# Kernel optimization log

Measured on AMD Instinct MI355X. Metric: run time of the kernel, lower is better.

The kernel has to match this reference:

```python
import jax, jax.numpy as jnp
import numpy as np

# ---- problem dims ----
B, S, C, H, W = 4, 8, 3, 256, 256
P = 68          # keypoints (self.points)
DS = 4          # detector downsample
WIN = 8
STEPS = 10      # Gauss-Newton iterations per frame pair
EPS = 1e-6
GRAY_W = jnp.array([0.299, 0.587, 0.114], dtype=jnp.float32)

# window offsets [K,2] in (x,y)
_rng = jnp.arange(-WIN, WIN + 1, dtype=jnp.float32)
_OFF = jnp.stack(jnp.meshgrid(_rng, _rng, indexing='xy'), -1).reshape(-1, 2)


def setup_inputs() -> dict:
    key = jax.random.key(0)
    k1, k2 = jax.random.split(key)
    inputs = jax.random.normal(k1, (B, S, C, H, W), dtype=jnp.float32)
    Wdet = jax.random.normal(k2, (P, C, 3, 3), dtype=jnp.float32) * 0.1
    bdet = jnp.zeros((P,), dtype=jnp.float32)
    return {"inputs": inputs, "Wdet": Wdet, "bdet": bdet}


def _bilinear(img, xy):
    # img [H,W]; xy [...,2] in (x,y) pixel coords -> sampled values [...]
    x = jnp.clip(xy[..., 0], 0.0, W - 1.001)
    y = jnp.clip(xy[..., 1], 0.0, H - 1.001)
    x0 = jnp.floor(x); y0 = jnp.floor(y)
    wx = x - x0; wy = y - y0
    x0i = x0.astype(jnp.int32); y0i = y0.astype(jnp.int32)
    x1i = jnp.minimum(x0i + 1, W - 1); y1i = jnp.minimum(y0i + 1, H - 1)
    v00 = img[y0i, x0i]; v01 = img[y0i, x1i]
    v10 = img[y1i, x0i]; v11 = img[y1i, x1i]
    return (1 - wy) * ((1 - wx) * v00 + wx * v01) + wy * ((1 - wx) * v10 + wx * v11)


def _grad_xy(img):
    # central differences with edge replication
    px = jnp.pad(img, ((0, 0), (1, 1)), mode='edge')
    py = jnp.pad(img, ((1, 1), (0, 0)), mode='edge')
    gx = (px[:, 2:] - px[:, :-2]) * 0.5
    gy = (py[2:, :] - py[:-2, :]) * 0.5
    return gx, gy


def _lk_track(old, new, pts):
    # one Lucas-Kanade tracking step: old/new [H,W] gray, pts [P,2] -> [P,2]
    gx, gy = _grad_xy(old)
    pos0 = pts[:, None, :] + _OFF[None]            # [P,K,2]
    I0 = _bilinear(old, pos0)                      # [P,K] template patch
    Ix = _bilinear(gx, pos0)
    Iy = _bilinear(gy, pos0)
    Gxx = (Ix * Ix).sum(-1); Gxy = (Ix * Iy).sum(-1); Gyy = (Iy * Iy).sum(-1)
    det = Gxx * Gyy - Gxy * Gxy + EPS
    Ginv = jnp.stack([jnp.stack([Gyy, -Gxy], -1),
                      jnp.stack([-Gxy, Gxx], -1)], -2) / det[:, None, None]  # [P,2,2]

    def step(i, v):
        I1 = _bilinear(new, pos0 + v[:, None, :])  # [P,K]
        err = I0 - I1
        b = jnp.stack([(err * Ix).sum(-1), (err * Iy).sum(-1)], -1)  # [P,2]
        return v + jnp.einsum('pij,pj->pi', Ginv, b)

    v = jax.lax.fori_loop(0, STEPS, step, jnp.zeros_like(pts))
    return pts + v


def _lk_forward_backward(gray, locs):
    # gray [S,H,W], locs [S,P,2] -> nextPts, fbackPts, backPts each [S,P,2]
    def f(pts, frames):
        o, n = frames
        q = _lk_track(o, n, pts)
        return q, q

    # forward: track detector locs of frame 0 through the sequence
    _, fout = jax.lax.scan(f, locs[0], (gray[:-1], gray[1:]))
    nextPts = jnp.concatenate([locs[:1], fout], 0)
    ro, rn = gray[1:][::-1], gray[:-1][::-1]
    # forward-backward: track the forward end point back to frame 0
    _, fbout = jax.lax.scan(f, nextPts[-1], (ro, rn))
    fbackPts = jnp.concatenate([nextPts[-1:], fbout], 0)[::-1]
    # backward: track detector locs of last frame back through the sequence
    _, bout = jax.lax.scan(f, locs[-1], (ro, rn))
    backPts = jnp.concatenate([locs[-1:], bout], 0)[::-1]
    return nextPts, fbackPts, backPts


def _detector(x, Wdet, bdet):
    # x [N,C,H,W] -> heatmaps [N,P,H/DS,W/DS], locs [N,P,2] (pixel coords), scores [N,P]
    hm = jax.lax.conv_general_dilated(
        x, Wdet, window_strides=(DS, DS), padding='SAME',
        dimension_numbers=('NCHW', 'OIHW', 'NCHW')) + bdet[None, :, None, None]
    N, _, Hd, Wd = hm.shape
    flat = hm.reshape(N, P, Hd * Wd)
    prob = jax.nn.softmax(flat, axis=-1)
    ys, xs = jnp.meshgrid(jnp.arange(Hd, dtype=hm.dtype),
                          jnp.arange(Wd, dtype=hm.dtype), indexing='ij')
    ex = (prob * xs.reshape(-1)).sum(-1) * DS   # soft-argmax, upscaled to input px
    ey = (prob * ys.reshape(-1)).sum(-1) * DS
    locs = jnp.stack([ex, ey], -1)
    scos = flat.max(-1)
    return hm, locs, scos


def reference(inputs, Wdet, bdet):
    x = inputs.reshape(B * S, C, H, W)
    hm, locs, scos = _detector(x, Wdet, bdet)
    heatmaps = hm.reshape(B, S, P, H // DS, W // DS)
    batch_locs = locs.reshape(B, S, P, 2)
    batch_scos = scos.reshape(B, S, P)
    gray = jnp.einsum('bschw,c->bshw', inputs, GRAY_W)  # [B,S,H,W]
    nextPts, fbackPts, backPts = jax.vmap(_lk_forward_backward)(gray, batch_locs)
    return heatmaps, batch_locs, batch_scos, nextPts, fbackPts, backPts
```

## Files before the change

kernel.cpp:

```cpp
#include <hip/hip_runtime.h>
#include <math.h>

namespace {
constexpr int Bn = 4, Sn = 8, Cn = 3, Himg = 256, Wimg = 256;
constexpr int Pn = 68, DS = 4, WIN = 8, STEPS = 10;
constexpr int HWi = Himg * Wimg;
constexpr int NIMG = Bn * Sn;
constexpr int HD = Himg / DS, WD = Wimg / DS;
constexpr int Kwin = (2 * WIN + 1) * (2 * WIN + 1);
}

__global__ __launch_bounds__(256) void gray2_kernel(const float* __restrict__ in,
                                                    float* __restrict__ gray,
                                                    float* __restrict__ sh) {
    int idx = blockIdx.x * blockDim.x + threadIdx.x;
    int total = NIMG * HWi / 4;
    if (idx >= total) return;
    int img = idx / (HWi / 4);
    int off = idx % (HWi / 4);
    const float* base = in + (size_t)img * 3 * HWi;
    float4 c0 = ((const float4*)(base))[off];
    float4 c1 = ((const float4*)(base + HWi))[off];
    float4 c2 = ((const float4*)(base + 2 * HWi))[off];
    float4 g;
    g.x = 0.299f * c0.x + 0.587f * c1.x + 0.114f * c2.x;
    g.y = 0.299f * c0.y + 0.587f * c1.y + 0.114f * c2.y;
    g.z = 0.299f * c0.z + 0.587f * c1.z + 0.114f * c2.z;
    g.w = 0.299f * c0.w + 0.587f * c1.w + 0.114f * c2.w;
    float gn = 0.f;
    int gi = idx * 4 + 4;
    if (gi < NIMG * HWi) {
        int i2 = gi / HWi;
        int o2 = gi % HWi;
        const float* b2 = in + (size_t)i2 * 3 * HWi;
        gn = 0.299f * b2[o2] + 0.587f * b2[o2 + HWi] + 0.114f * b2[o2 + 2 * HWi];
    }
    ((float4*)(gray + (size_t)img * HWi))[off] = g;
    float4 s;
    s.x = g.y; s.y = g.z; s.z = g.w; s.w = gn;
    ((float4*)(sh + (size_t)img * HWi))[off] = s;
}

__global__ __launch_bounds__(256) void conv_kernel(const float* __restrict__ x,
                                                   const float* __restrict__ Wdet,
                                                   const float* __restrict__ bdet,
                                                   float* __restrict__ hm) {
    __shared__ float wsh[Pn * 27];
    __shared__ float bsh[Pn];
    __shared__ float insh[3][3][Wimg];
    int n = blockIdx.x >> 6;
    int oy = blockIdx.x & 63;
    int tid = threadIdx.x;
    for (int t = tid; t < Pn * 27; t += 256) wsh[t] = Wdet[t];
    if (tid < Pn) bsh[tid] = bdet[tid];
    for (int t = tid; t < 3 * 3 * Wimg; t += 256) {
        int c = t / (3 * Wimg);
        int r = (t / Wimg) % 3;
        int col = t % Wimg;
        insh[c][r][col] = x[(size_t)n * 3 * HWi + (size_t)c * HWi + (oy * 4 + r) * Wimg + col];
    }
    __syncthreads();
    int ox = tid & 63;
    int wid = tid >> 6;
    float in_reg[27];
    #pragma unroll
    for (int c = 0; c < 3; c++)
        #pragma unroll
        for (int ky = 0; ky < 3; ky++)
            #pragma unroll
            for (int kx = 0; kx < 3; kx++)
                in_reg[c * 9 + ky * 3 + kx] = insh[c][ky][ox * 4 + kx];
    #pragma unroll
    for (int i = 0; i < 17; i++) {
        int p = wid + i * 4;
        const float* w = &wsh[p * 27];
        float acc = bsh[p];
        #pragma unroll
        for (int j = 0; j < 27; j++) acc += w[j] * in_reg[j];
        hm[(size_t)n * Pn * 4096 + (size_t)p * 4096 + oy * 64 + ox] = acc;
    }
}

__global__ __launch_bounds__(256) void smax_kernel(const float* __restrict__ hm,
                                                   float* __restrict__ locs,
                                                   float* __restrict__ scos) {
    int row = blockIdx.x;
    const float4* r = (const float4*)(hm + (size_t)row * 4096);
    int tid = threadIdx.x;
    float v[16];
    #pragma unroll
    for (int j = 0; j < 4; j++) {
        float4 q = r[tid + 256 * j];
        v[4 * j + 0] = q.x; v[4 * j + 1] = q.y; v[4 * j + 2] = q.z; v[4 * j + 3] = q.w;
    }
    float m = v[0];
    #pragma unroll
    for (int i = 1; i < 16; i++) m = fmaxf(m, v[i]);
    __shared__ float redm[4];
    #pragma unroll
    for (int o = 32; o; o >>= 1) m = fmaxf(m, __shfl_xor(m, o, 64));
    int wid = tid >> 6, lane = tid & 63;
    if (lane == 0) redm[wid] = m;
    __syncthreads();
    m = fmaxf(fmaxf(redm[0], redm[1]), fmaxf(redm[2], redm[3]));
    float s = 0.f, sx = 0.f, sy = 0.f;
    #pragma unroll
    for (int j = 0; j < 4; j++) {
        #pragma unroll
        for (int q = 0; q < 4; q++) {
            int e = (tid + 256 * j) * 4 + q;
            float ev = expf(v[4 * j + q] - m);
            s += ev;
            sx += ev * (float)(e & 63);
            sy += ev * (float)(e >> 6);
        }
    }
    #pragma unroll
    for (int o = 32; o; o >>= 1) {
        s  += __shfl_xor(s, o, 64);
        sx += __shfl_xor(sx, o, 64);
        sy += __shfl_xor(sy, o, 64);
    }
    __shared__ float reds[3][4];
    if (lane == 0) { reds[0][wid] = s; reds[1][wid] = sx; reds[2][wid] = sy; }
    __syncthreads();
    if (tid == 0) {
        float S_ = reds[0][0] + reds[0][1] + reds[0][2] + reds[0][3];
        float SX = reds[1][0] + reds[1][1] + reds[1][2] + reds[1][3];
        float SY = reds[2][0] + reds[2][1] + reds[2][2] + reds[2][3];
        locs[(size_t)row * 2 + 0] = SX / S_ * 4.0f;
        locs[(size_t)row * 2 + 1] = SY / S_ * 4.0f;
        scos[row] = m;
    }
}

template <int CTRL>
__device__ inline float dpp_add(float v) {
    int t = __builtin_amdgcn_update_dpp(0, __builtin_bit_cast(int, v), CTRL, 0xF, 0xF, true);
    return v + __builtin_bit_cast(float, t);
}

__device__ inline float wredw(float v) {
    v = dpp_add<0x111>(v);
    v = dpp_add<0x112>(v);
    v = dpp_add<0x114>(v);
    v = dpp_add<0x118>(v);
    v = dpp_add<0x142>(v);
    v = dpp_add<0x143>(v);
    int s = __builtin_amdgcn_readlane(__builtin_bit_cast(int, v), 63);
    return __builtin_bit_cast(float, s);
}

__device__ void lk_track_pair(const float* __restrict__ oldI, const float* __restrict__ oldS,
                              const float* __restrict__ newI, const float* __restrict__ newS,
                              float& px, float& py, const float* dxs, const float* dys,
                              float s4w) {
    const float XM = (float)(Wimg - 1.001);
    const float YM = (float)(Himg - 1.001);
    float I0[5], Ix[5], Iy[5], qx[5], qy[5];
    {
        float wx[5], wy[5];
        const float* pb[5];
        int xe[5], am[5], a0[5], a1[5], ap[5], xm[5], xp[5];
        #pragma unroll
        for (int j = 0; j < 5; j++) {
            qx[j] = px + dxs[j];
            qy[j] = py + dys[j];
            float x = fminf(fmaxf(qx[j], 0.0f), XM);
            float y = fminf(fmaxf(qy[j], 0.0f), YM);
            float x0f = floorf(x), y0f = floorf(y);
            wx[j] = x - x0f; wy[j] = y - y0f;
            int xi = (int)x0f, yi = (int)y0f;
            xe[j] = xi & ~1;
            pb[j] = (xi & 1) ? oldS : oldI;
            xm[j] = max(xi - 1, 0);
            xp[j] = min(xi + 2, Wimg - 1);
            a0[j] = yi * Wimg;
            a1[j] = a0[j] + Wimg;
            am[j] = max(yi - 1, 0) * Wimg;
            ap[j] = min(yi + 2, Himg - 1) * Wimg;
        }
        float2 Pm[5], P0[5], P1[5], Pp[5];
        float c0m[5], c0p[5], c1m[5], c1p[5];
        #pragma unroll
        for (int j = 0; j < 5; j++) {
            Pm[j] = *(const float2*)(pb[j] + am[j] + xe[j]);
            P0[j] = *(const float2*)(pb[j] + a0[j] + xe[j]);
            P1[j] = *(const float2*)(pb[j] + a1[j] + xe[j]);
            Pp[j] = *(const float2*)(pb[j] + ap[j] + xe[j]);
            c0m[j] = oldI[a0[j] + xm[j]];
            c0p[j] = oldI[a0[j] + xp[j]];
            c1m[j] = oldI[a1[j] + xm[j]];
            c1p[j] = oldI[a1[j] + xp[j]];
        }
        #pragma unroll
        for (int j = 0; j < 5; j++) {
            float m0 = Pm[j].x, m1 = Pm[j].y;
            float c00 = P0[j].x, c01 = P0[j].y;
            float c10 = P1[j].x, c11 = P1[j].y;
            float p0 = Pp[j].x, p1 = Pp[j].y;
            float u = 1.0f - wx[j], t = 1.0f - wy[j];
            I0[j] = t * (u * c00 + wx[j] * c01) + wy[j] * (u * c10 + wx[j] * c11);
            float gx00 = 0.5f * (c01 - c0m[j]);
            float gx01 = 0.5f * (c0p[j] - c00);
            float gx10 = 0.5f * (c11 - c1m[j]);
            float gx11 = 0.5f * (c1p[j] - c10);
            Ix[j] = t * (u * gx00 + wx[j] * gx01) + wy[j] * (u * gx10 + wx[j] * gx11);
            float gy00 = 0.5f * (c10 - m0);
            float gy01 = 0.5f * (c11 - m1);
            float gy10 = 0.5f * (p0 - c00);
            float gy11 = 0.5f * (p1 - c01);
            Iy[j] = t * (u * gy00 + wx[j] * gy01) + wy[j] * (u * gy10 + wx[j] * gy11);
        }
        Ix[4] *= s4w;
        Iy[4] *= s4w;
    }
    float gxx = 0.f, gxy = 0.f, gyy = 0.f;
    #pragma unroll
    for (int j = 0; j < 5; j++) { gxx += Ix[j] * Ix[j]; gxy += Ix[j] * Iy[j]; gyy += Iy[j] * Iy[j]; }
    gxx = wredw(gxx); gxy = wredw(gxy); gyy = wredw(gyy);
    float det = gxx * gyy - gxy * gxy + 1e-6f;
    float A = gyy / det, Bv = -gxy / det, D = gxx / det;
    float vx = 0.f, vy = 0.f;
    for (int it = 0; it < STEPS; ++it) {
        float fx[5], fy[5];
        const float* pb[5];
        int aa[5];
        #pragma unroll
        for (int j = 0; j < 5; j++) {
            float x = fminf(fmaxf(qx[j] + vx, 0.0f), XM);
            float y = fminf(fmaxf(qy[j] + vy, 0.0f), YM);
            float x0f = floorf(x), y0f = floorf(y);
            fx[j] = x - x0f; fy[j] = y - y0f;
            int xi = (int)x0f, yi = (int)y0f;
            pb[j] = (xi & 1) ? newS : newI;
            aa[j] = yi * Wimg + (xi & ~1);
        }
        float2 R0[5], R1[5];
        #pragma unroll
        for (int j = 0; j < 5; j++) {
            R0[j] = *(const float2*)(pb[j] + aa[j]);
            R1[j] = *(const float2*)(pb[j] + aa[j] + Wimg);
        }
        float bx = 0.f, by = 0.f;
        #pragma unroll
        for (int j = 0; j < 5; j++) {
            float u = 1.0f - fx[j], t = 1.0f - fy[j];
            float I1 = t * (u * R0[j].x + fx[j] * R0[j].y) + fy[j] * (u * R1[j].x + fx[j] * R1[j].y);
            float err = I0[j] - I1;
            bx += err * Ix[j];
            by += err * Iy[j];
        }
        bx = wredw(bx); by = wredw(by);
        vx += A * bx + Bv * by;
        vy += Bv * bx + D * by;
    }
    px += vx; py += vy;
}

__global__ __launch_bounds__(64) void lk_pair_kernel(const float* __restrict__ gray,
                                                     const float* __restrict__ sh,
                                                     const float* __restrict__ locs,
                                                     float* __restrict__ nextPts,
                                                     float* __restrict__ fbackPts,
                                                     float* __restrict__ backPts) {
    int g = blockIdx.x;
    int typ = g / (Bn * Pn);
    int r = g % (Bn * Pn);
    int b = r / Pn;
    int p = r % Pn;
    int lane = threadIdx.x;
    const float* G = gray + (size_t)b * Sn * HWi;
    const float* S = sh + (size_t)b * Sn * HWi;
    float dxs[5], dys[5];
    #pragma unroll
    for (int j = 0; j < 4; j++) {
        int k = lane + 64 * j;
        dxs[j] = (float)(k % 17 - 8);
        dys[j] = (float)(k / 17 - 8);
    }
    {
        int k4 = (lane < Kwin - 256) ? 256 + lane : 256;
        dxs[4] = (float)(k4 % 17 - 8);
        dys[4] = (float)(k4 / 17 - 8);
    }
    float s4w = (lane < Kwin - 256) ? 1.0f : 0.0f;
    auto LIDX = [&](int s) { return (((size_t)b * Sn + s) * Pn + p) * 2; };
    if (typ == 0) {
        float px = locs[LIDX(0)], py = locs[LIDX(0) + 1];
        if (lane == 0) { nextPts[LIDX(0)] = px; nextPts[LIDX(0) + 1] = py; }
        for (int s = 0; s < 7; s++) {
            lk_track_pair(G + s * HWi, S + s * HWi, G + (s + 1) * HWi, S + (s + 1) * HWi,
                          px, py, dxs, dys, s4w);
            if (lane == 0) { nextPts[LIDX(s + 1)] = px; nextPts[LIDX(s + 1) + 1] = py; }
        }
        if (lane == 0) { fbackPts[LIDX(7)] = px; fbackPts[LIDX(7) + 1] = py; }
        for (int i = 0; i < 7; i++) {
            lk_track_pair(G + (7 - i) * HWi, S + (7 - i) * HWi, G + (6 - i) * HWi, S + (6 - i) * HWi,
                          px, py, dxs, dys, s4w);
            if (lane == 0) { fbackPts[LIDX(6 - i)] = px; fbackPts[LIDX(6 - i) + 1] = py; }
        }
    } else {
        float px = locs[LIDX(7)], py = locs[LIDX(7) + 1];
        if (lane == 0) { backPts[LIDX(7)] = px; backPts[LIDX(7) + 1] = py; }
        for (int i = 0; i < 7; i++) {
            lk_track_pair(G + (7 - i) * HWi, S + (7 - i) * HWi, G + (6 - i) * HWi, S + (6 - i) * HWi,
                          px, py, dxs, dys, s4w);
            if (lane == 0) { backPts[LIDX(6 - i)] = px; backPts[LIDX(6 - i) + 1] = py; }
        }
    }
}

__device__ inline float px_fly(const float* __restrict__ im, int idx) {
    return 0.299f * im[idx] + 0.587f * im[idx + HWi] + 0.114f * im[idx + 2 * HWi];
}

__device__ void lk_track_fly(const float* __restrict__ oldI, const float* __restrict__ newI,
                             float& px, float& py, const float* dxs, const float* dys,
                             float s4w) {
    const float XM = (float)(Wimg - 1.001);
    const float YM = (float)(Himg - 1.001);
    float I0[5], Ix[5], Iy[5], qx[5], qy[5];
    {
        float wx[5], wy[5];
        int am[5], a0[5], a1[5], ap[5], xm[5], x0[5], x1[5], xp[5];
        #pragma unroll
        for (int j = 0; j < 5; j++) {
            qx[j] = px + dxs[j]; qy[j] = py + dys[j];
            float x = fminf(fmaxf(qx[j], 0.0f), XM);
            float y = fminf(fmaxf(qy[j], 0.0f), YM);
            float x0f = floorf(x), y0f = floorf(y);
            wx[j] = x - x0f; wy[j] = y - y0f;
            int xi = (int)x0f, yi = (int)y0f;
            x0[j] = xi; x1[j] = min(xi + 1, Wimg - 1);
            xm[j] = max(xi - 1, 0); xp[j] = min(xi + 2, Wimg - 1);
            a0[j] = yi * Wimg;
            a1[j] = min(yi + 1, Himg - 1) * Wimg;
            am[j] = max(yi - 1, 0) * Wimg;
            ap[j] = min(yi + 2, Himg - 1) * Wimg;
        }
        #pragma unroll
        for (int j = 0; j < 5; j++) {
            float m0 = px_fly(oldI, am[j] + x0[j]), m1 = px_fly(oldI, am[j] + x1[j]);
            float c0m = px_fly(oldI, a0[j] + xm[j]), c00 = px_fly(oldI, a0[j] + x0[j]);
            float c01 = px_fly(oldI, a0[j] + x1[j]), c0p = px_fly(oldI, a0[j] + xp[j]);
            float c1m = px_fly(oldI, a1[j] + xm[j]), c10 = px_fly(oldI, a1[j] + x0[j]);
            float c11 = px_fly(oldI, a1[j] + x1[j]), c1p = px_fly(oldI, a1[j] + xp[j]);
            float p0 = px_fly(oldI, ap[j] + x0[j]), p1 = px_fly(oldI, ap[j] + x1[j]);
            float u = 1.0f - wx[j], t = 1.0f - wy[j];
            I0[j] = t * (u * c00 + wx[j] * c01) + wy[j] * (u * c10 + wx[j] * c11);
            Ix[j] = t * (u * 0.5f * (c01 - c0m) + wx[j] * 0.5f * (c0p - c00))
                  + wy[j] * (u * 0.5f * (c11 - c1m) + wx[j] * 0.5f * (c1p - c10));
            Iy[j] = t * (u * 0.5f * (c10 - m0) + wx[j] * 0.5f * (c11 - m1))
                  + wy[j] * (u * 0.5f * (p0 - c00) + wx[j] * 0.5f * (p1 - c01));
        }
        Ix[4] *= s4w; Iy[4] *= s4w;
    }
    float gxx = 0.f, gxy = 0.f, gyy = 0.f;
    #pragma unroll
    for (int j = 0; j < 5; j++) { gxx += Ix[j] * Ix[j]; gxy += Ix[j] * Iy[j]; gyy += Iy[j] * Iy[j]; }
    gxx = wredw(gxx); gxy = wredw(gxy); gyy = wredw(gyy);
    float det = gxx * gyy - gxy * gxy + 1e-6f;
    float A = gyy / det, Bv = -gxy / det, D = gxx / det;
    float vx = 0.f, vy = 0.f;
    for (int it = 0; it < STEPS; ++it) {
        float bx = 0.f, by = 0.f;
        #pragma unroll
        for (int j = 0; j < 5; j++) {
            float x = fminf(fmaxf(qx[j] + vx, 0.0f), XM);
            float y = fminf(fmaxf(qy[j] + vy, 0.0f), YM);
            float x0f = floorf(x), y0f = floorf(y);
            float fxx = x - x0f, fyy = y - y0f;
            int xi = (int)x0f, yi = (int)y0f;
            int ad = yi * Wimg + xi;
            float v00 = px_fly(newI, ad), v01 = px_fly(newI, ad + 1);
            float v10 = px_fly(newI, ad + Wimg), v11 = px_fly(newI, ad + Wimg + 1);
            float u = 1.0f - fxx, t = 1.0f - fyy;
            float I1 = t * (u * v00 + fxx * v01) + fyy * (u * v10 + fxx * v11);
            float err = I0[j] - I1;
            bx += err * Ix[j];
            by += err * Iy[j];
        }
        bx = wredw(bx); by = wredw(by);
        vx += A * bx + Bv * by;
        vy += Bv * bx + D * by;
    }
    px += vx; py += vy;
}

__global__ __launch_bounds__(64) void lk_fly_kernel(const float* __restrict__ in,
                                                    const float* __restrict__ locs,
                                                    float* __restrict__ nextPts,
                                                    float* __restrict__ fbackPts,
                                                    float* __restrict__ backPts) {
    constexpr size_t FS = (size_t)3 * HWi;
    int g = blockIdx.x;
    int typ = g / (Bn * Pn);
    int r = g % (Bn * Pn);
    int b = r / Pn;
    int p = r % Pn;
    int lane = threadIdx.x;
    const float* G = in + (size_t)b * Sn * FS;
    float dxs[5], dys[5];
    #pragma unroll
    for (int j = 0; j < 4; j++) {
        int k = lane + 64 * j;
        dxs[j] = (float)(k % 17 - 8);
        dys[j] = (float)(k / 17 - 8);
    }
    {
        int k4 = (lane < Kwin - 256) ? 256 + lane : 256;
        dxs[4] = (float)(k4 % 17 - 8);
        dys[4] = (float)(k4 / 17 - 8);
    }
    float s4w = (lane < Kwin - 256) ? 1.0f : 0.0f;
    auto LIDX = [&](int s) { return (((size_t)b * Sn + s) * Pn + p) * 2; };
    if (typ == 0) {
        float px = locs[LIDX(0)], py = locs[LIDX(0) + 1];
        if (lane == 0) { nextPts[LIDX(0)] = px; nextPts[LIDX(0) + 1] = py; }
        for (int s = 0; s < 7; s++) {
            lk_track_fly(G + s * FS, G + (s + 1) * FS, px, py, dxs, dys, s4w);
            if (lane == 0) { nextPts[LIDX(s + 1)] = px; nextPts[LIDX(s + 1) + 1] = py; }
        }
        if (lane == 0) { fbackPts[LIDX(7)] = px; fbackPts[LIDX(7) + 1] = py; }
        for (int i = 0; i < 7; i++) {
            lk_track_fly(G + (7 - i) * FS, G + (6 - i) * FS, px, py, dxs, dys, s4w);
            if (lane == 0) { fbackPts[LIDX(6 - i)] = px; fbackPts[LIDX(6 - i) + 1] = py; }
        }
    } else {
        float px = locs[LIDX(7)], py = locs[LIDX(7) + 1];
        if (lane == 0) { backPts[LIDX(7)] = px; backPts[LIDX(7) + 1] = py; }
        for (int i = 0; i < 7; i++) {
            lk_track_fly(G + (7 - i) * FS, G + (6 - i) * FS, px, py, dxs, dys, s4w);
            if (lane == 0) { backPts[LIDX(6 - i)] = px; backPts[LIDX(6 - i) + 1] = py; }
        }
    }
}

extern "C" void kernel_launch(void* const* d_in, const int* in_sizes, int n_in,
                              void* d_out, int out_size, void* d_ws, size_t ws_size,
                              hipStream_t stream) {
    const float* inputs = (const float*)d_in[0];
    const float* Wdet = (const float*)d_in[1];
    const float* bdet = (const float*)d_in[2];
    float* out = (float*)d_out;

    const size_t N_hm = (size_t)Bn * Sn * Pn * HD * WD;
    const size_t N_pts = (size_t)Bn * Sn * Pn * 2;
    float* hm = out;
    float* locs = out + N_hm;
    float* scos = locs + N_pts;
    float* nextPts = scos + (size_t)Bn * Sn * Pn;
    float* fbackPts = nextPts + N_pts;
    float* backPts = fbackPts + N_pts;

    conv_kernel<<<NIMG * 64, 256, 0, stream>>>(inputs, Wdet, bdet, hm);
    smax_kernel<<<NIMG * Pn, 256, 0, stream>>>(hm, locs, scos);

    const size_t gray_elems = (size_t)NIMG * HWi;
    if (ws_size >= 2 * gray_elems * sizeof(float)) {
        float* gray = (float*)d_ws;
        float* sh = gray + gray_elems;
        gray2_kernel<<<(NIMG * HWi / 4 + 255) / 256, 256, 0, stream>>>(inputs, gray, sh);
        lk_pair_kernel<<<2 * Bn * Pn, 64, 0, stream>>>(gray, sh, locs, nextPts, fbackPts, backPts);
    } else {
        lk_fly_kernel<<<2 * Bn * Pn, 64, 0, stream>>>(inputs, locs, nextPts, fbackPts, backPts);
    }
}
```

Measured before the change: 121.7 us.

## Stage per-frame 40x40 LK patches in LDS instead of shifted gray copies

The gray kernel no longer writes a second, one-pixel-shifted gray image, which halves the workspace traffic. Each LK track step now cooperatively loads a 40x40 window of the old and new frames into shared memory. Template, gradient and Gauss-Newton samples are then read from LDS, with a fallback to global reads when the displaced window leaves the patch. This trades global gathers for one bulk patch load and two barriers per frame pair. The fly path also gains edge clamping on the +1 neighbours.

New measurement: 125.3 us. 1.03x slower.

```diff
diff --git a/kernel.cpp b/kernel.cpp
--- a/kernel.cpp
+++ b/kernel.cpp
@@ -8,11 +8,13 @@
 constexpr int NIMG = Bn * Sn;
 constexpr int HD = Himg / DS, WD = Wimg / DS;
 constexpr int Kwin = (2 * WIN + 1) * (2 * WIN + 1);
-}
-
-__global__ __launch_bounds__(256) void gray2_kernel(const float* __restrict__ in,
-                                                    float* __restrict__ gray,
-                                                    float* __restrict__ sh) {
+constexpr int PS = 40;
+constexpr int PIT = 41;
+constexpr int HP = 19;
+}
+
+__global__ __launch_bounds__(256) void gray_kernel(const float* __restrict__ in,
+                                                   float* __restrict__ gray) {
     int idx = blockIdx.x * blockDim.x + threadIdx.x;
     int total = NIMG * HWi / 4;
     if (idx >= total) return;
@@ -27,18 +29,7 @@
     g.y = 0.299f * c0.y + 0.587f * c1.y + 0.114f * c2.y;
     g.z = 0.299f * c0.z + 0.587f * c1.z + 0.114f * c2.z;
     g.w = 0.299f * c0.w + 0.587f * c1.w + 0.114f * c2.w;
-    float gn = 0.f;
-    int gi = idx * 4 + 4;
-    if (gi < NIMG * HWi) {
-        int i2 = gi / HWi;
-        int o2 = gi % HWi;
-        const float* b2 = in + (size_t)i2 * 3 * HWi;
-        gn = 0.299f * b2[o2] + 0.587f * b2[o2 + HWi] + 0.114f * b2[o2 + 2 * HWi];
-    }
     ((float4*)(gray + (size_t)img * HWi))[off] = g;
-    float4 s;
-    s.x = g.y; s.y = g.z; s.z = g.w; s.w = gn;
-    ((float4*)(sh + (size_t)img * HWi))[off] = s;
 }
 
 __global__ __launch_bounds__(256) void conv_kernel(const float* __restrict__ x,
@@ -151,65 +142,70 @@
     return __builtin_bit_cast(float, s);
 }
 
-__device__ void lk_track_pair(const float* __restrict__ oldI, const float* __restrict__ oldS,
-                              const float* __restrict__ newI, const float* __restrict__ newS,
-                              float& px, float& py, const float* dxs, const float* dys,
-                              float s4w) {
+__device__ void lk_track_patch(const float* __restrict__ oldI, const float* __restrict__ newI,
+                               float* __restrict__ oldP, float* __restrict__ newP,
+                               float& px, float& py, const float* dxs, const float* dys,
+                               float s4w, int lane) {
     const float XM = (float)(Wimg - 1.001);
     const float YM = (float)(Himg - 1.001);
+    int cx0 = min(max((int)floorf(px), 0), 255) - HP;
+    int cy0 = min(max((int)floorf(py), 0), 255) - HP;
+    __syncthreads();
+    #pragma unroll
+    for (int i = 0; i < 25; i++) {
+        int idx = lane + 64 * i;
+        int rr = idx / PS;
+        int cc = idx - rr * PS;
+        int gr = min(max(cy0 + rr, 0), 255);
+        int gc = min(max(cx0 + cc, 0), 255);
+        int ga = gr * Wimg + gc;
+        oldP[rr * PIT + cc] = oldI[ga];
+        newP[rr * PIT + cc] = newI[ga];
+    }
+    __syncthreads();
     float I0[5], Ix[5], Iy[5], qx[5], qy[5];
     {
         float wx[5], wy[5];
-        const float* pb[5];
-        int xe[5], am[5], a0[5], a1[5], ap[5], xm[5], xp[5];
+        int base[5];
         #pragma unroll
         for (int j = 0; j < 5; j++) {
             qx[j] = px + dxs[j];
             qy[j] = py + dys[j];
             float x = fminf(fmaxf(qx[j], 0.0f), XM);
             float y = fminf(fmaxf(qy[j], 0.0f), YM);
-            float x0f = floorf(x), y0f = floorf(y);
-            wx[j] = x - x0f; wy[j] = y - y0f;
-            int xi = (int)x0f, yi = (int)y0f;
-            xe[j] = xi & ~1;
-            pb[j] = (xi & 1) ? oldS : oldI;
-            xm[j] = max(xi - 1, 0);
-            xp[j] = min(xi + 2, Wimg - 1);
-            a0[j] = yi * Wimg;
-            a1[j] = a0[j] + Wimg;
-            am[j] = max(yi - 1, 0) * Wimg;
-            ap[j] = min(yi + 2, Himg - 1) * Wimg;
-        }
-        float2 Pm[5], P0[5], P1[5], Pp[5];
-        float c0m[5], c0p[5], c1m[5], c1p[5];
-        #pragma unroll
-        for (int j = 0; j < 5; j++) {
-            Pm[j] = *(const float2*)(pb[j] + am[j] + xe[j]);
-            P0[j] = *(const float2*)(pb[j] + a0[j] + xe[j]);
-            P1[j] = *(const float2*)(pb[j] + a1[j] + xe[j]);
-            Pp[j] = *(const float2*)(pb[j] + ap[j] + xe[j]);
-            c0m[j] = oldI[a0[j] + xm[j]];
-            c0p[j] = oldI[a0[j] + xp[j]];
-            c1m[j] = oldI[a1[j] + xm[j]];
-            c1p[j] = oldI[a1[j] + xp[j]];
-        }
-        #pragma unroll
-        for (int j = 0; j < 5; j++) {
-            float m0 = Pm[j].x, m1 = Pm[j].y;
-            float c00 = P0[j].x, c01 = P0[j].y;
-            float c10 = P1[j].x, c11 = P1[j].y;
-            float p0 = Pp[j].x, p1 = Pp[j].y;
+            float xf = floorf(x), yf = floorf(y);
+            wx[j] = x - xf; wy[j] = y - yf;
+            base[j] = ((int)yf - cy0) * PIT + ((int)xf - cx0);
+        }
+        float m0[5], m1[5], c0m[5], c00[5], c01[5], c0p[5], c1m[5], c10[5], c11[5], c1p[5], p0[5], p1[5];
+        #pragma unroll
+        for (int j = 0; j < 5; j++) {
+            m0[j]  = oldP[base[j] - PIT];
+            m1[j]  = oldP[base[j] - PIT + 1];
+            c0m[j] = oldP[base[j] - 1];
+            c00[j] = oldP[base[j]];
+            c01[j] = oldP[base[j] + 1];
+            c0p[j] = oldP[base[j] + 2];
+            c1m[j] = oldP[base[j] + PIT - 1];
+            c10[j] = oldP[base[j] + PIT];
+            c11[j] = oldP[base[j] + PIT + 1];
+            c1p[j] = oldP[base[j] + PIT + 2];
+            p0[j]  = oldP[base[j] + 2 * PIT];
+            p1[j]  = oldP[base[j] + 2 * PIT + 1];
+        }
+        #pragma unroll
+        for (int j = 0; j < 5; j++) {
             float u = 1.0f - wx[j], t = 1.0f - wy[j];
-            I0[j] = t * (u * c00 + wx[j] * c01) + wy[j] * (u * c10 + wx[j] * c11);
-            float gx00 = 0.5f * (c01 - c0m[j]);
-            float gx01 = 0.5f * (c0p[j] - c00);
-            float gx10 = 0.5f * (c11 - c1m[j]);
-            float gx11 = 0.5f * (c1p[j] - c10);
+            I0[j] = t * (u * c00[j] + wx[j] * c01[j]) + wy[j] * (u * c10[j] + wx[j] * c11[j]);
+            float gx00 = 0.5f * (c01[j] - c0m[j]);
+            float gx01 = 0.5f * (c0p[j] - c00[j]);
+            float gx10 = 0.5f * (c11[j] - c1m[j]);
+            float gx11 = 0.5f * (c1p[j] - c10[j]);
             Ix[j] = t * (u * gx00 + wx[j] * gx01) + wy[j] * (u * gx10 + wx[j] * gx11);
-            float gy00 = 0.5f * (c10 - m0);
-            float gy01 = 0.5f * (c11 - m1);
-            float gy10 = 0.5f * (p0 - c00);
-            float gy11 = 0.5f * (p1 - c01);
+            float gy00 = 0.5f * (c10[j] - m0[j]);
+            float gy01 = 0.5f * (c11[j] - m1[j]);
+            float gy10 = 0.5f * (p0[j] - c00[j]);
+            float gy11 = 0.5f * (p1[j] - c01[j]);
             Iy[j] = t * (u * gy00 + wx[j] * gy01) + wy[j] * (u * gy10 + wx[j] * gy11);
         }
         Ix[4] *= s4w;
@@ -223,30 +219,53 @@
     float A = gyy / det, Bv = -gxy / det, D = gxx / det;
     float vx = 0.f, vy = 0.f;
     for (int it = 0; it < STEPS; ++it) {
-        float fx[5], fy[5];
-        const float* pb[5];
-        int aa[5];
-        #pragma unroll
-        for (int j = 0; j < 5; j++) {
-            float x = fminf(fmaxf(qx[j] + vx, 0.0f), XM);
-            float y = fminf(fmaxf(qy[j] + vy, 0.0f), YM);
-            float x0f = floorf(x), y0f = floorf(y);
-            fx[j] = x - x0f; fy[j] = y - y0f;
-            int xi = (int)x0f, yi = (int)y0f;
-            pb[j] = (xi & 1) ? newS : newI;
-            aa[j] = yi * Wimg + (xi & ~1);
-        }
-        float2 R0[5], R1[5];
-        #pragma unroll
-        for (int j = 0; j < 5; j++) {
-            R0[j] = *(const float2*)(pb[j] + aa[j]);
-            R1[j] = *(const float2*)(pb[j] + aa[j] + Wimg);
+        float lox = fminf(fmaxf(px - 8.0f + vx, 0.0f), XM);
+        float hix = fminf(fmaxf(px + 8.0f + vx, 0.0f), XM);
+        float loy = fminf(fmaxf(py - 8.0f + vy, 0.0f), YM);
+        float hiy = fminf(fmaxf(py + 8.0f + vy, 0.0f), YM);
+        int lx = (int)floorf(lox) - cx0, hx = (int)floorf(hix) - cx0;
+        int ly = (int)floorf(loy) - cy0, hy = (int)floorf(hiy) - cy0;
+        bool fast = (lx >= 0) & (hx <= PS - 2) & (ly >= 0) & (hy <= PS - 2);
+        float fx[5], fy[5], v00[5], v01[5], v10[5], v11[5];
+        if (fast) {
+            int bb[5];
+            #pragma unroll
+            for (int j = 0; j < 5; j++) {
+                float x = fminf(fmaxf(qx[j] + vx, 0.0f), XM);
+                float y = fminf(fmaxf(qy[j] + vy, 0.0f), YM);
+                float xf = floorf(x), yf = floorf(y);
+                fx[j] = x - xf; fy[j] = y - yf;
+                bb[j] = ((int)yf - cy0) * PIT + ((int)xf - cx0);
+            }
+            #pragma unroll
+            for (int j = 0; j < 5; j++) {
+                v00[j] = newP[bb[j]];
+                v01[j] = newP[bb[j] + 1];
+                v10[j] = newP[bb[j] + PIT];
+                v11[j] = newP[bb[j] + PIT + 1];
+            }
+        } else {
+            #pragma unroll
+            for (int j = 0; j < 5; j++) {
+                float x = fminf(fmaxf(qx[j] + vx, 0.0f), XM);
+                float y = fminf(fmaxf(qy[j] + vy, 0.0f), YM);
+                float xf = floorf(x), yf = floorf(y);
+                fx[j] = x - xf; fy[j] = y - yf;
+                int xi = (int)xf, yi = (int)yf;
+                int ad = yi * Wimg + xi;
+                int d1 = (xi < Wimg - 1) ? 1 : 0;
+                int d2 = (yi < Himg - 1) ? Wimg : 0;
+                v00[j] = newI[ad];
+                v01[j] = newI[ad + d1];
+                v10[j] = newI[ad + d2];
+                v11[j] = newI[ad + d2 + d1];
+            }
         }
         float bx = 0.f, by = 0.f;
         #pragma unroll
         for (int j = 0; j < 5; j++) {
             float u = 1.0f - fx[j], t = 1.0f - fy[j];
-            float I1 = t * (u * R0[j].x + fx[j] * R0[j].y) + fy[j] * (u * R1[j].x + fx[j] * R1[j].y);
+            float I1 = t * (u * v00[j] + fx[j] * v01[j]) + fy[j] * (u * v10[j] + fx[j] * v11[j]);
             float err = I0[j] - I1;
             bx += err * Ix[j];
             by += err * Iy[j];
@@ -258,12 +277,13 @@
     px += vx; py += vy;
 }
 
-__global__ __launch_bounds__(64) void lk_pair_kernel(const float* __restrict__ gray,
-                                                     const float* __restrict__ sh,
-                                                     const float* __restrict__ locs,
-                                                     float* __restrict__ nextPts,
-                                                     float* __restrict__ fbackPts,
-                                                     float* __restrict__ backPts) {
+__global__ __launch_bounds__(64) void lk_patch_kernel(const float* __restrict__ gray,
+                                                      const float* __restrict__ locs,
+                                                      float* __restrict__ nextPts,
+                                                      float* __restrict__ fbackPts,
+                                                      float* __restrict__ backPts) {
+    __shared__ float oldP[PS * PIT];
+    __shared__ float newP[PS * PIT];
     int g = blockIdx.x;
     int typ = g / (Bn * Pn);
     int r = g % (Bn * Pn);
@@ -271,7 +291,6 @@
     int p = r % Pn;
     int lane = threadIdx.x;
     const float* G = gray + (size_t)b * Sn * HWi;
-    const float* S = sh + (size_t)b * Sn * HWi;
     float dxs[5], dys[5];
     #pragma unroll
     for (int j = 0; j < 4; j++) {
@@ -290,22 +309,19 @@
         float px = locs[LIDX(0)], py = locs[LIDX(0) + 1];
         if (lane == 0) { nextPts[LIDX(0)] = px; nextPts[LIDX(0) + 1] = py; }
         for (int s = 0; s < 7; s++) {
-            lk_track_pair(G + s * HWi, S + s * HWi, G + (s + 1) * HWi, S + (s + 1) * HWi,
-                          px, py, dxs, dys, s4w);
+            lk_track_patch(G + s * HWi, G + (s + 1) * HWi, oldP, newP, px, py, dxs, dys, s4w, lane);
             if (lane == 0) { nextPts[LIDX(s + 1)] = px; nextPts[LIDX(s + 1) + 1] = py; }
         }
         if (lane == 0) { fbackPts[LIDX(7)] = px; fbackPts[LIDX(7) + 1] = py; }
         for (int i = 0; i < 7; i++) {
-            lk_track_pair(G + (7 - i) * HWi, S + (7 - i) * HWi, G + (6 - i) * HWi, S + (6 - i) * HWi,
-                          px, py, dxs, dys, s4w);
+            lk_track_patch(G + (7 - i) * HWi, G + (6 - i) * HWi, oldP, newP, px, py, dxs, dys, s4w, lane);
             if (lane == 0) { fbackPts[LIDX(6 - i)] = px; fbackPts[LIDX(6 - i) + 1] = py; }
         }
     } else {
         float px = locs[LIDX(7)], py = locs[LIDX(7) + 1];
         if (lane == 0) { backPts[LIDX(7)] = px; backPts[LIDX(7) + 1] = py; }
         for (int i = 0; i < 7; i++) {
-            lk_track_pair(G + (7 - i) * HWi, S + (7 - i) * HWi, G + (6 - i) * HWi, S + (6 - i) * HWi,
-                          px, py, dxs, dys, s4w);
+            lk_track_patch(G + (7 - i) * HWi, G + (6 - i) * HWi, oldP, newP, px, py, dxs, dys, s4w, lane);
             if (lane == 0) { backPts[LIDX(6 - i)] = px; backPts[LIDX(6 - i) + 1] = py; }
         }
     }
@@ -373,8 +389,10 @@
             float fxx = x - x0f, fyy = y - y0f;
             int xi = (int)x0f, yi = (int)y0f;
             int ad = yi * Wimg + xi;
-            float v00 = px_fly(newI, ad), v01 = px_fly(newI, ad + 1);
-            float v10 = px_fly(newI, ad + Wimg), v11 = px_fly(newI, ad + Wimg + 1);
+            int d1 = (xi < Wimg - 1) ? 1 : 0;
+            int d2 = (yi < Himg - 1) ? Wimg : 0;
+            float v00 = px_fly(newI, ad), v01 = px_fly(newI, ad + d1);
+            float v10 = px_fly(newI, ad + d2), v11 = px_fly(newI, ad + d2 + d1);
             float u = 1.0f - fxx, t = 1.0f - fyy;
             float I1 = t * (u * v00 + fxx * v01) + fyy * (u * v10 + fxx * v11);
             float err = I0[j] - I1;
@@ -457,12 +475,11 @@
     conv_kernel<<<NIMG * 64, 256, 0, stream>>>(inputs, Wdet, bdet, hm);
     smax_kernel<<<NIMG * Pn, 256, 0, stream>>>(hm, locs, scos);
 
-    const size_t gray_elems = (size_t)NIMG * HWi;
-    if (ws_size >= 2 * gray_elems * sizeof(float)) {
+    const size_t gray_bytes = (size_t)NIMG * HWi * sizeof(float);
+    if (ws_size >= gray_bytes) {
         float* gray = (float*)d_ws;
-        float* sh = gray + gray_elems;
-        gray2_kernel<<<(NIMG * HWi / 4 + 255) / 256, 256, 0, stream>>>(inputs, gray, sh);
-        lk_pair_kernel<<<2 * Bn * Pn, 64, 0, stream>>>(gray, sh, locs, nextPts, fbackPts, backPts);
+        gray_kernel<<<(NIMG * HWi / 4 + 255) / 256, 256, 0, stream>>>(inputs, gray);
+        lk_patch_kernel<<<2 * Bn * Pn, 64, 0, stream>>>(gray, locs, nextPts, fbackPts, backPts);
     } else {
         lk_fly_kernel<<<2 * Bn * Pn, 64, 0, stream>>>(inputs, locs, nextPts, fbackPts, backPts);
     }
```

## Pack gray frames as vertical pairs so each bilinear tap is one float4 load

Applied to the files above, without the earlier changes.

Adds a preprocessing kernel that stores each gray frame as float2 (row, row+1) pairs, plus a copy shifted by one column. Each bilinear 2x2 footprint then becomes a single aligned float4 load, and the gradient stencil needs only a few extra loads. A new LK kernel uses this layout for both template setup and the Gauss-Newton iterations. The cost is a workspace twice as large as before, written by the new preprocessing pass. The change also clamps the neighbour offsets in the fallback path.

Measured after the change: 113.3 us. 1.07x faster.

```diff
diff --git a/kernel.cpp b/kernel.cpp
--- a/kernel.cpp
+++ b/kernel.cpp
@@ -8,6 +8,289 @@
 constexpr int NIMG = Bn * Sn;
 constexpr int HD = Himg / DS, WD = Wimg / DS;
 constexpr int Kwin = (2 * WIN + 1) * (2 * WIN + 1);
+constexpr int P2ROWS = 257;
+constexpr int P2FR = P2ROWS * 256;
+constexpr int NSHIFT = NIMG * P2FR;
+}
+
+__global__ __launch_bounds__(256) void conv_kernel(const float* __restrict__ x,
+                                                   const float* __restrict__ Wdet,
+                                                   const float* __restrict__ bdet,
+                                                   float* __restrict__ hm) {
+    __shared__ float wsh[Pn * 27];
+    __shared__ float bsh[Pn];
+    __shared__ float insh[3][3][Wimg];
+    int n = blockIdx.x >> 6;
+    int oy = blockIdx.x & 63;
+    int tid = threadIdx.x;
+    for (int t = tid; t < Pn * 27; t += 256) wsh[t] = Wdet[t];
+    if (tid < Pn) bsh[tid] = bdet[tid];
+    for (int t = tid; t < 3 * 3 * Wimg; t += 256) {
+        int c = t / (3 * Wimg);
+        int r = (t / Wimg) % 3;
+        int col = t % Wimg;
+        insh[c][r][col] = x[(size_t)n * 3 * HWi + (size_t)c * HWi + (oy * 4 + r) * Wimg + col];
+    }
+    __syncthreads();
+    int ox = tid & 63;
+    int wid = tid >> 6;
+    float in_reg[27];
+    #pragma unroll
+    for (int c = 0; c < 3; c++)
+        #pragma unroll
+        for (int ky = 0; ky < 3; ky++)
+            #pragma unroll
+            for (int kx = 0; kx < 3; kx++)
+                in_reg[c * 9 + ky * 3 + kx] = insh[c][ky][ox * 4 + kx];
+    #pragma unroll
+    for (int i = 0; i < 17; i++) {
+        int p = wid + i * 4;
+        const float* w = &wsh[p * 27];
+        float acc = bsh[p];
+        #pragma unroll
+        for (int j = 0; j < 27; j++) acc += w[j] * in_reg[j];
+        hm[(size_t)n * Pn * 4096 + (size_t)p * 4096 + oy * 64 + ox] = acc;
+    }
+}
+
+__global__ __launch_bounds__(256) void smax_kernel(const float* __restrict__ hm,
+                                                   float* __restrict__ locs,
+                                                   float* __restrict__ scos) {
+    int row = blockIdx.x;
+    const float4* r = (const float4*)(hm + (size_t)row * 4096);
+    int tid = threadIdx.x;
+    float v[16];
+    #pragma unroll
+    for (int j = 0; j < 4; j++) {
+        float4 q = r[tid + 256 * j];
+        v[4 * j + 0] = q.x; v[4 * j + 1] = q.y; v[4 * j + 2] = q.z; v[4 * j + 3] = q.w;
+    }
+    float m = v[0];
+    #pragma unroll
+    for (int i = 1; i < 16; i++) m = fmaxf(m, v[i]);
+    __shared__ float redm[4];
+    #pragma unroll
+    for (int o = 32; o; o >>= 1) m = fmaxf(m, __shfl_xor(m, o, 64));
+    int wid = tid >> 6, lane = tid & 63;
+    if (lane == 0) redm[wid] = m;
+    __syncthreads();
+    m = fmaxf(fmaxf(redm[0], redm[1]), fmaxf(redm[2], redm[3]));
+    float s = 0.f, sx = 0.f, sy = 0.f;
+    #pragma unroll
+    for (int j = 0; j < 4; j++) {
+        #pragma unroll
+        for (int q = 0; q < 4; q++) {
+            int e = (tid + 256 * j) * 4 + q;
+            float ev = expf(v[4 * j + q] - m);
+            s += ev;
+            sx += ev * (float)(e & 63);
+            sy += ev * (float)(e >> 6);
+        }
+    }
+    #pragma unroll
+    for (int o = 32; o; o >>= 1) {
+        s  += __shfl_xor(s, o, 64);
+        sx += __shfl_xor(sx, o, 64);
+        sy += __shfl_xor(sy, o, 64);
+    }
+    __shared__ float reds[3][4];
+    if (lane == 0) { reds[0][wid] = s; reds[1][wid] = sx; reds[2][wid] = sy; }
+    __syncthreads();
+    if (tid == 0) {
+        float S_ = reds[0][0] + reds[0][1] + reds[0][2] + reds[0][3];
+        float SX = reds[1][0] + reds[1][1] + reds[1][2] + reds[1][3];
+        float SY = reds[2][0] + reds[2][1] + reds[2][2] + reds[2][3];
+        locs[(size_t)row * 2 + 0] = SX / S_ * 4.0f;
+        locs[(size_t)row * 2 + 1] = SY / S_ * 4.0f;
+        scos[row] = m;
+    }
+}
+
+__global__ __launch_bounds__(256) void grayP2_kernel(const float* __restrict__ in,
+                                                     float2* __restrict__ P2r,
+                                                     float2* __restrict__ P2rs) {
+    __shared__ float g[9][257];
+    int blk = blockIdx.x;
+    int n = blk / 33, q = blk % 33;
+    int tid = threadIdx.x;
+    const float* base = in + (size_t)n * 3 * HWi;
+    #pragma unroll
+    for (int r = 0; r < 9; r++) {
+        int row = min(max(8 * q - 1 + r, 0), 255);
+        int a = row * Wimg + tid;
+        g[r][tid] = 0.299f * base[a] + 0.587f * base[a + HWi] + 0.114f * base[a + 2 * HWi];
+    }
+    if (tid < 9) g[tid][256] = g[tid][255];
+    __syncthreads();
+    float2* pr = P2r + (size_t)n * P2FR;
+    float2* ps = P2rs + (size_t)n * P2FR;
+    #pragma unroll
+    for (int j = 0; j < 8; j++) {
+        int k = 8 * q + j;
+        if (k <= 256) {
+            float a = g[j][tid], b = g[j + 1][tid];
+            pr[k * 256 + tid] = make_float2(a, b);
+            float a2 = g[j][tid + 1], b2 = g[j + 1][tid + 1];
+            ps[k * 256 + tid] = make_float2(a2, b2);
+        }
+    }
+}
+
+template <int CTRL>
+__device__ inline float dpp_add(float v) {
+    int t = __builtin_amdgcn_update_dpp(0, __builtin_bit_cast(int, v), CTRL, 0xF, 0xF, true);
+    return v + __builtin_bit_cast(float, t);
+}
+
+__device__ inline float wredw(float v) {
+    v = dpp_add<0x111>(v);
+    v = dpp_add<0x112>(v);
+    v = dpp_add<0x114>(v);
+    v = dpp_add<0x118>(v);
+    v = dpp_add<0x142>(v);
+    v = dpp_add<0x143>(v);
+    int s = __builtin_amdgcn_readlane(__builtin_bit_cast(int, v), 63);
+    return __builtin_bit_cast(float, s);
+}
+
+__device__ void lk_track_p2(const float2* __restrict__ Po, const float2* __restrict__ Pn,
+                            float& px, float& py, const float* dxs, const float* dys,
+                            float s4w) {
+    const float XM = (float)(Wimg - 1.001);
+    const float YM = (float)(Himg - 1.001);
+    float I0[5], Ix[5], Iy[5], qx[5], qy[5];
+    {
+        float wx[5], wy[5];
+        int idx[5], sb[5], xm[5], xp[5];
+        #pragma unroll
+        for (int j = 0; j < 5; j++) {
+            qx[j] = px + dxs[j];
+            qy[j] = py + dys[j];
+            float x = fminf(fmaxf(qx[j], 0.0f), XM);
+            float y = fminf(fmaxf(qy[j], 0.0f), YM);
+            float xf = floorf(x), yf = floorf(y);
+            wx[j] = x - xf; wy[j] = y - yf;
+            int xi = (int)xf, yi = (int)yf;
+            int col = xi & ~1;
+            idx[j] = yi * 256 + col + ((xi & 1) ? NSHIFT : 0);
+            sb[j] = (yi + 1) * 256;
+            xm[j] = max(xi - 1, 0);
+            xp[j] = min(xi + 2, Wimg - 1);
+        }
+        float4 A[5], B[5];
+        float2 S1[5], S2[5];
+        #pragma unroll
+        for (int j = 0; j < 5; j++) {
+            A[j] = *reinterpret_cast<const float4*>(Po + idx[j]);
+            B[j] = *reinterpret_cast<const float4*>(Po + idx[j] + 512);
+            S1[j] = Po[sb[j] + xm[j]];
+            S2[j] = Po[sb[j] + xp[j]];
+        }
+        #pragma unroll
+        for (int j = 0; j < 5; j++) {
+            float m0 = A[j].x, c00 = A[j].y, m1 = A[j].z, c01 = A[j].w;
+            float c10 = B[j].x, p0 = B[j].y, c11 = B[j].z, p1 = B[j].w;
+            float c0m = S1[j].x, c1m = S1[j].y, c0p = S2[j].x, c1p = S2[j].y;
+            float u = 1.0f - wx[j], t = 1.0f - wy[j];
+            I0[j] = t * (u * c00 + wx[j] * c01) + wy[j] * (u * c10 + wx[j] * c11);
+            float gx00 = 0.5f * (c01 - c0m);
+            float gx01 = 0.5f * (c0p - c00);
+            float gx10 = 0.5f * (c11 - c1m);
+            float gx11 = 0.5f * (c1p - c10);
+            Ix[j] = t * (u * gx00 + wx[j] * gx01) + wy[j] * (u * gx10 + wx[j] * gx11);
+            float gy00 = 0.5f * (c10 - m0);
+            float gy01 = 0.5f * (c11 - m1);
+            float gy10 = 0.5f * (p0 - c00);
+            float gy11 = 0.5f * (p1 - c01);
+            Iy[j] = t * (u * gy00 + wx[j] * gy01) + wy[j] * (u * gy10 + wx[j] * gy11);
+        }
+        Ix[4] *= s4w;
+        Iy[4] *= s4w;
+    }
+    float gxx = 0.f, gxy = 0.f, gyy = 0.f;
+    #pragma unroll
+    for (int j = 0; j < 5; j++) { gxx += Ix[j] * Ix[j]; gxy += Ix[j] * Iy[j]; gyy += Iy[j] * Iy[j]; }
+    gxx = wredw(gxx); gxy = wredw(gxy); gyy = wredw(gyy);
+    float det = gxx * gyy - gxy * gxy + 1e-6f;
+    float A = gyy / det, Bv = -gxy / det, D = gxx / det;
+    float vx = 0.f, vy = 0.f;
+    for (int it = 0; it < STEPS; ++it) {
+        float fx[5], fy[5];
+        int id[5];
+        #pragma unroll
+        for (int j = 0; j < 5; j++) {
+            float x = fminf(fmaxf(qx[j] + vx, 0.0f), XM);
+            float y = fminf(fmaxf(qy[j] + vy, 0.0f), YM);
+            float xf = floorf(x), yf = floorf(y);
+            fx[j] = x - xf; fy[j] = y - yf;
+            int xi = (int)xf, yi = (int)yf;
+            id[j] = (yi + 1) * 256 + (xi & ~1) + ((xi & 1) ? NSHIFT : 0);
+        }
+        float4 Q[5];
+        #pragma unroll
+        for (int j = 0; j < 5; j++) Q[j] = *reinterpret_cast<const float4*>(Pn + id[j]);
+        float bx = 0.f, by = 0.f;
+        #pragma unroll
+        for (int j = 0; j < 5; j++) {
+            float u = 1.0f - fx[j], t = 1.0f - fy[j];
+            float I1 = t * (u * Q[j].x + fx[j] * Q[j].z) + fy[j] * (u * Q[j].y + fx[j] * Q[j].w);
+            float err = I0[j] - I1;
+            bx += err * Ix[j];
+            by += err * Iy[j];
+        }
+        bx = wredw(bx); by = wredw(by);
+        vx += A * bx + Bv * by;
+        vy += Bv * bx + D * by;
+    }
+    px += vx; py += vy;
+}
+
+__global__ __launch_bounds__(64) void lk_p2_kernel(const float2* __restrict__ P2r,
+                                                   const float* __restrict__ locs,
+                                                   float* __restrict__ nextPts,
+                                                   float* __restrict__ fbackPts,
+                                                   float* __restrict__ backPts) {
+    int g = blockIdx.x;
+    int typ = g / (Bn * Pn);
+    int r = g % (Bn * Pn);
+    int b = r / Pn;
+    int p = r % Pn;
+    int lane = threadIdx.x;
+    const float2* F = P2r + (size_t)b * Sn * P2FR;
+    float dxs[5], dys[5];
+    #pragma unroll
+    for (int j = 0; j < 4; j++) {
+        int k = lane + 64 * j;
+        dxs[j] = (float)(k % 17 - 8);
+        dys[j] = (float)(k / 17 - 8);
+    }
+    {
+        int k4 = (lane < Kwin - 256) ? 256 + lane : 256;
+        dxs[4] = (float)(k4 % 17 - 8);
+        dys[4] = (float)(k4 / 17 - 8);
+    }
+    float s4w = (lane < Kwin - 256) ? 1.0f : 0.0f;
+    auto LIDX = [&](int s) { return (((size_t)b * Sn + s) * Pn + p) * 2; };
+    if (typ == 0) {
+        float px = locs[LIDX(0)], py = locs[LIDX(0) + 1];
+        if (lane == 0) { nextPts[LIDX(0)] = px; nextPts[LIDX(0) + 1] = py; }
+        for (int s = 0; s < 7; s++) {
+            lk_track_p2(F + s * P2FR, F + (s + 1) * P2FR, px, py, dxs, dys, s4w);
+            if (lane == 0) { nextPts[LIDX(s + 1)] = px; nextPts[LIDX(s + 1) + 1] = py; }
+        }
+        if (lane == 0) { fbackPts[LIDX(7)] = px; fbackPts[LIDX(7) + 1] = py; }
+        for (int i = 0; i < 7; i++) {
+            lk_track_p2(F + (7 - i) * P2FR, F + (6 - i) * P2FR, px, py, dxs, dys, s4w);
+            if (lane == 0) { fbackPts[LIDX(6 - i)] = px; fbackPts[LIDX(6 - i) + 1] = py; }
+        }
+    } else {
+        float px = locs[LIDX(7)], py = locs[LIDX(7) + 1];
+        if (lane == 0) { backPts[LIDX(7)] = px; backPts[LIDX(7) + 1] = py; }
+        for (int i = 0; i < 7; i++) {
+            lk_track_p2(F + (7 - i) * P2FR, F + (6 - i) * P2FR, px, py, dxs, dys, s4w);
+            if (lane == 0) { backPts[LIDX(6 - i)] = px; backPts[LIDX(6 - i) + 1] = py; }
+        }
+    }
 }
 
 __global__ __launch_bounds__(256) void gray2_kernel(const float* __restrict__ in,
@@ -41,116 +324,6 @@
     ((float4*)(sh + (size_t)img * HWi))[off] = s;
 }
 
-__global__ __launch_bounds__(256) void conv_kernel(const float* __restrict__ x,
-                                                   const float* __restrict__ Wdet,
-                                                   const float* __restrict__ bdet,
-                                                   float* __restrict__ hm) {
-    __shared__ float wsh[Pn * 27];
-    __shared__ float bsh[Pn];
-    __shared__ float insh[3][3][Wimg];
-    int n = blockIdx.x >> 6;
-    int oy = blockIdx.x & 63;
-    int tid = threadIdx.x;
-    for (int t = tid; t < Pn * 27; t += 256) wsh[t] = Wdet[t];
-    if (tid < Pn) bsh[tid] = bdet[tid];
-    for (int t = tid; t < 3 * 3 * Wimg; t += 256) {
-        int c = t / (3 * Wimg);
-        int r = (t / Wimg) % 3;
-        int col = t % Wimg;
-        insh[c][r][col] = x[(size_t)n * 3 * HWi + (size_t)c * HWi + (oy * 4 + r) * Wimg + col];
-    }
-    __syncthreads();
-    int ox = tid & 63;
-    int wid = tid >> 6;
-    float in_reg[27];
-    #pragma unroll
-    for (int c = 0; c < 3; c++)
-        #pragma unroll
-        for (int ky = 0; ky < 3; ky++)
-            #pragma unroll
-            for (int kx = 0; kx < 3; kx++)
-                in_reg[c * 9 + ky * 3 + kx] = insh[c][ky][ox * 4 + kx];
-    #pragma unroll
-    for (int i = 0; i < 17; i++) {
-        int p = wid + i * 4;
-        const float* w = &wsh[p * 27];
-        float acc = bsh[p];
-        #pragma unroll
-        for (int j = 0; j < 27; j++) acc += w[j] * in_reg[j];
-        hm[(size_t)n * Pn * 4096 + (size_t)p * 4096 + oy * 64 + ox] = acc;
-    }
-}
-
-__global__ __launch_bounds__(256) void smax_kernel(const float* __restrict__ hm,
-                                                   float* __restrict__ locs,
-                                                   float* __restrict__ scos) {
-    int row = blockIdx.x;
-    const float4* r = (const float4*)(hm + (size_t)row * 4096);
-    int tid = threadIdx.x;
-    float v[16];
-    #pragma unroll
-    for (int j = 0; j < 4; j++) {
-        float4 q = r[tid + 256 * j];
-        v[4 * j + 0] = q.x; v[4 * j + 1] = q.y; v[4 * j + 2] = q.z; v[4 * j + 3] = q.w;
-    }
-    float m = v[0];
-    #pragma unroll
-    for (int i = 1; i < 16; i++) m = fmaxf(m, v[i]);
-    __shared__ float redm[4];
-    #pragma unroll
-    for (int o = 32; o; o >>= 1) m = fmaxf(m, __shfl_xor(m, o, 64));
-    int wid = tid >> 6, lane = tid & 63;
-    if (lane == 0) redm[wid] = m;
-    __syncthreads();
-    m = fmaxf(fmaxf(redm[0], redm[1]), fmaxf(redm[2], redm[3]));
-    float s = 0.f, sx = 0.f, sy = 0.f;
-    #pragma unroll
-    for (int j = 0; j < 4; j++) {
-        #pragma unroll
-        for (int q = 0; q < 4; q++) {
-            int e = (tid + 256 * j) * 4 + q;
-            float ev = expf(v[4 * j + q] - m);
-            s += ev;
-            sx += ev * (float)(e & 63);
-            sy += ev * (float)(e >> 6);
-        }
-    }
-    #pragma unroll
-    for (int o = 32; o; o >>= 1) {
-        s  += __shfl_xor(s, o, 64);
-        sx += __shfl_xor(sx, o, 64);
-        sy += __shfl_xor(sy, o, 64);
-    }
-    __shared__ float reds[3][4];
-    if (lane == 0) { reds[0][wid] = s; reds[1][wid] = sx; reds[2][wid] = sy; }
-    __syncthreads();
-    if (tid == 0) {
-        float S_ = reds[0][0] + reds[0][1] + reds[0][2] + reds[0][3];
-        float SX = reds[1][0] + reds[1][1] + reds[1][2] + reds[1][3];
-        float SY = reds[2][0] + reds[2][1] + reds[2][2] + reds[2][3];
-        locs[(size_t)row * 2 + 0] = SX / S_ * 4.0f;
-        locs[(size_t)row * 2 + 1] = SY / S_ * 4.0f;
-        scos[row] = m;
-    }
-}
-
-template <int CTRL>
-__device__ inline float dpp_add(float v) {
-    int t = __builtin_amdgcn_update_dpp(0, __builtin_bit_cast(int, v), CTRL, 0xF, 0xF, true);
-    return v + __builtin_bit_cast(float, t);
-}
-
-__device__ inline float wredw(float v) {
-    v = dpp_add<0x111>(v);
-    v = dpp_add<0x112>(v);
-    v = dpp_add<0x114>(v);
-    v = dpp_add<0x118>(v);
-    v = dpp_add<0x142>(v);
-    v = dpp_add<0x143>(v);
-    int s = __builtin_amdgcn_readlane(__builtin_bit_cast(int, v), 63);
-    return __builtin_bit_cast(float, s);
-}
-
 __device__ void lk_track_pair(const float* __restrict__ oldI, const float* __restrict__ oldS,
                               const float* __restrict__ newI, const float* __restrict__ newS,
                               float& px, float& py, const float* dxs, const float* dys,
@@ -373,8 +546,10 @@
             float fxx = x - x0f, fyy = y - y0f;
             int xi = (int)x0f, yi = (int)y0f;
             int ad = yi * Wimg + xi;
-            float v00 = px_fly(newI, ad), v01 = px_fly(newI, ad + 1);
-            float v10 = px_fly(newI, ad + Wimg), v11 = px_fly(newI, ad + Wimg + 1);
+            int d1 = (xi < Wimg - 1) ? 1 : 0;
+            int d2 = (yi < Himg - 1) ? Wimg : 0;
+            float v00 = px_fly(newI, ad), v01 = px_fly(newI, ad + d1);
+            float v10 = px_fly(newI, ad + d2), v11 = px_fly(newI, ad + d2 + d1);
             float u = 1.0f - fxx, t = 1.0f - fyy;
             float I1 = t * (u * v00 + fxx * v01) + fyy * (u * v10 + fxx * v11);
             float err = I0[j] - I1;
@@ -457,8 +632,14 @@
     conv_kernel<<<NIMG * 64, 256, 0, stream>>>(inputs, Wdet, bdet, hm);
     smax_kernel<<<NIMG * Pn, 256, 0, stream>>>(hm, locs, scos);
 
+    const size_t p2_bytes = (size_t)2 * NIMG * P2FR * sizeof(float2);
     const size_t gray_elems = (size_t)NIMG * HWi;
-    if (ws_size >= 2 * gray_elems * sizeof(float)) {
+    if (ws_size >= p2_bytes) {
+        float2* P2r = (float2*)d_ws;
+        float2* P2rs = P2r + (size_t)NIMG * P2FR;
+        grayP2_kernel<<<NIMG * 33, 256, 0, stream>>>(inputs, P2r, P2rs);
+        lk_p2_kernel<<<2 * Bn * Pn, 64, 0, stream>>>(P2r, locs, nextPts, fbackPts, backPts);
+    } else if (ws_size >= 2 * gray_elems * sizeof(float)) {
         float* gray = (float*)d_ws;
         float* sh = gray + gray_elems;
         gray2_kernel<<<(NIMG * HWi / 4 + 255) / 256, 256, 0, stream>>>(inputs, gray, sh);
```
